# Kernel tuning notes

Hardware: AMD Instinct MI355X
Metric: run time of the kernel (lower is better)

Reference implementation:

```python
import jax, jax.numpy as jnp
import numpy as np

DT = 0.1
K = 262144


def _skew(v):
    # v: [k,3] -> [k,3,3]
    x, y, z = v[..., 0], v[..., 1], v[..., 2]
    O = jnp.zeros_like(x)
    return jnp.stack([
        jnp.stack([O, -z, y], -1),
        jnp.stack([z, O, -x], -1),
        jnp.stack([-y, x, O], -1)], -2)


def _se3_exp(t):
    # t: [k,6] twist = [rho(linear), phi(angular)] -> (R [k,3,3], p [k,3])
    rho, phi = t[:, :3], t[:, 3:]
    th2 = jnp.sum(phi * phi, -1)
    small = th2 < 1e-8
    th2s = jnp.where(small, 1.0, th2)        # safe denominator
    th = jnp.sqrt(th2s)
    A = jnp.where(small, 1.0 - th2 / 6.0, jnp.sin(th) / th)
    B = jnp.where(small, 0.5 - th2 / 24.0, (1.0 - jnp.cos(th)) / th2s)
    C = jnp.where(small, 1.0 / 6.0 - th2 / 120.0, (th - jnp.sin(th)) / (th2s * th))
    S = _skew(phi)
    S2 = S @ S
    I = jnp.eye(3, dtype=t.dtype)
    R = I + A[:, None, None] * S + B[:, None, None] * S2
    V = I + B[:, None, None] * S + C[:, None, None] * S2
    p = jnp.einsum('kij,kj->ki', V, rho)
    return R, p


def _adjoint(R, p):
    # SE3 adjoint for twist order [linear, angular]: [[R, [p]x R],[0, R]]
    top = jnp.concatenate([R, _skew(p) @ R], -1)
    bot = jnp.concatenate([jnp.zeros_like(R), R], -1)
    return jnp.concatenate([top, bot], -2)  # [k,6,6]


def setup_inputs() -> dict:
    key = jax.random.key(0)
    ks = jax.random.split(key, 8)
    s = jax.random.normal(ks[0], (K, 1, 18), dtype=jnp.float32) * 0.1
    # state layout: [pos(3), rot(9), twist(6)]; rotation must be a valid R (identity, as in fake_state)
    s = s.at[:, :, 3:12].set(jnp.eye(3, dtype=jnp.float32).reshape(9))
    a = jax.random.normal(ks[1], (K, 1, 6), dtype=jnp.float32) * 0.1
    h0 = jnp.zeros((1, K, 12), dtype=jnp.float32)
    W_ih = jax.random.normal(ks[2], (12, 21), dtype=jnp.float32) / np.sqrt(21)
    W_hh = jax.random.normal(ks[3], (12, 12), dtype=jnp.float32) / np.sqrt(12)
    W1 = jax.random.normal(ks[4], (128, 12), dtype=jnp.float32) / np.sqrt(12)
    W2 = jax.random.normal(ks[5], (128, 128), dtype=jnp.float32) / np.sqrt(128)
    W3 = jax.random.normal(ks[6], (6, 128), dtype=jnp.float32) / np.sqrt(128)
    return {"s": s, "a": a, "h0": h0, "W_ih": W_ih, "W_hh": W_hh, "W1": W1, "W2": W2, "W3": W3}


def reference(s, a, h0, W_ih, W_hh, W1, W2, W3):
    k = s.shape[0]
    # RNN input: pose-rot+vel (cols 3:) concat action -> [k, 21] (tau=1)
    x = jnp.concatenate([s[:, :, 3:], a], -1)[:, 0]
    h1 = jnp.tanh(x @ W_ih.T + h0[0] @ W_hh.T)          # [k,12] single RNN step, no bias
    hN = h1[None]                                        # [1,k,12]
    lrelu = lambda z: jnp.where(z >= 0, z, 0.1 * z)
    dv = lrelu(lrelu(h1 @ W1.T) @ W2.T) @ W3.T           # [k,6]
    v = s[:, -1, -6:]                                    # body twist
    p = s[:, -1, :3]
    R = s[:, -1, 3:12].reshape(k, 3, 3)
    # SE3 integration: M_next = M_current @ Exp(v*dt)
    Re, pe = _se3_exp(v * DT)
    R_next = R @ Re
    p_next = jnp.einsum('kij,kj->ki', R, pe) + p
    # M_next^-1
    Rinv = jnp.swapaxes(R_next, -1, -2)
    pinv = -jnp.einsum('kij,kj->ki', Rinv, p_next)
    # velocity update through adjoints
    vI = jnp.einsum('kij,kj->ki', _adjoint(R, p), v)
    v_next = jnp.einsum('kij,kj->ki', _adjoint(Rinv, pinv), vI + dv)
    s_next = jnp.concatenate([p_next, R_next.reshape(k, 9), v_next], -1)[:, None, :]
    return s_next, hN, dv
```

## Files before the change

### kernel.cpp

```cpp
#include <hip/hip_runtime.h>
#include <math.h>

typedef __attribute__((ext_vector_type(8))) short short8;
typedef __attribute__((ext_vector_type(4))) float f32x4;

#define DT_STEP 0.1f

static __device__ __forceinline__ unsigned bf16rne(float f) {
    unsigned u = __builtin_bit_cast(unsigned, f);
    return (u + 0x7fffu + ((u >> 16) & 1u)) >> 16;
}
static __device__ __forceinline__ unsigned short bf16pk1(float f) {
    unsigned r;
    asm("v_cvt_pk_bf16_f32 %0, %1, %1" : "=v"(r) : "v"(f));
    return (unsigned short)r;
}
static __device__ __forceinline__ unsigned bf16pk2(float lo, float hi) {
    unsigned r;
    asm("v_cvt_pk_bf16_f32 %0, %1, %2" : "=v"(r) : "v"(lo), "v"(hi));
    return r;
}
static __device__ __forceinline__ float tanh_fast(float v) {
    float e = __expf(2.0f * v);
    return 1.0f - 2.0f / (e + 1.0f);
}

static __device__ __forceinline__ void mm3(const float* A, const float* B, float* C) {
#pragma unroll
    for (int i = 0; i < 3; ++i)
#pragma unroll
        for (int j = 0; j < 3; ++j)
            C[i * 3 + j] = A[i * 3 + 0] * B[0 * 3 + j] + A[i * 3 + 1] * B[1 * 3 + j] + A[i * 3 + 2] * B[2 * 3 + j];
}
static __device__ __forceinline__ void mv3(const float* A, const float* x, float* y) {
#pragma unroll
    for (int i = 0; i < 3; ++i) y[i] = A[i * 3 + 0] * x[0] + A[i * 3 + 1] * x[1] + A[i * 3 + 2] * x[2];
}
static __device__ __forceinline__ void mtv3(const float* A, const float* x, float* y) {
#pragma unroll
    for (int i = 0; i < 3; ++i) y[i] = A[0 * 3 + i] * x[0] + A[1 * 3 + i] * x[1] + A[2 * 3 + i] * x[2];
}
static __device__ __forceinline__ void cross3(const float* p, const float* u, float* y) {
    y[0] = p[1] * u[2] - p[2] * u[1];
    y[1] = p[2] * u[0] - p[0] * u[2];
    y[2] = p[0] * u[1] - p[1] * u[0];
}

__global__ __launch_bounds__(256)
void weights_prep(const float* __restrict__ W1, const float* __restrict__ W2,
                  const float* __restrict__ W3, unsigned short* __restrict__ ws) {
    int i = blockIdx.x * 256 + threadIdx.x;
    if (i < 4096) {
        int n = i >> 5, k = i & 31;
        ws[i] = (k < 12) ? (unsigned short)bf16rne(W1[n * 12 + k]) : (unsigned short)0;
    } else if (i < 20480) {
        ws[i] = (unsigned short)bf16rne(W2[i - 4096]);
    } else if (i < 22528) {
        int j = i - 20480;
        int jj = j & 7;
        int l = (j >> 3) & 15;
        int kl = j >> 7;
        int k = kl * 8 + jj;
        ws[i] = (l < 6) ? (unsigned short)bf16rne(W3[l * 128 + k]) : (unsigned short)0;
    }
}

__global__ __launch_bounds__(256, 2)
void auv_mfma4_kernel(const float* __restrict__ s, const float* __restrict__ a,
                      const float* __restrict__ h0, const float* __restrict__ W_ih,
                      const float* __restrict__ W_hh, const unsigned short* __restrict__ Wbf,
                      float* __restrict__ out, int K)
{
    __shared__ __align__(16) char lds[4][18432];
    const int tid  = threadIdx.x;
    const int wid  = tid >> 6;
    const int lane = tid & 63;
    const int l15  = lane & 15;
    const int lg   = lane >> 4;

    char* base = &lds[wid][0];
    char* h1t  = base;
    char* l12  = base + 2048;
    char* dvt  = h1t;

    const unsigned short* W1A = Wbf;
    const unsigned short* W2B = Wbf + 4096;
    const unsigned short* W3B = Wbf + 20480;

    const int e_raw = blockIdx.x * 256 + wid * 64 + lane;
    const int e  = e_raw < K ? e_raw : K - 1;
    const bool live = e_raw < K;

    const float* srow = s  + (size_t)e * 18;
    const float* arow = a  + (size_t)e * 6;
    const float* hrow = h0 + (size_t)e * 12;

    float xv[21];
#pragma unroll
    for (int i = 0; i < 15; ++i) xv[i] = srow[3 + i];
#pragma unroll
    for (int i = 0; i < 6; ++i)  xv[15 + i] = arow[i];
    float h0v[12];
#pragma unroll
    for (int i = 0; i < 12; ++i) h0v[i] = hrow[i];

    float h1v[12];
#pragma unroll
    for (int j = 0; j < 12; ++j) {
        float acc = 0.f;
        const float* wih = W_ih + j * 21;
#pragma unroll
        for (int i = 0; i < 21; ++i) acc = fmaf(wih[i], xv[i], acc);
        const float* whh = W_hh + j * 12;
#pragma unroll
        for (int i = 0; i < 12; ++i) acc = fmaf(whh[i], h0v[i], acc);
        h1v[j] = tanh_fast(acc);
    }

    if (live) {
        float4* h4 = (float4*)(out + (size_t)K * 18 + (size_t)e * 12);
        h4[0] = make_float4(h1v[0], h1v[1], h1v[2], h1v[3]);
        h4[1] = make_float4(h1v[4], h1v[5], h1v[6], h1v[7]);
        h4[2] = make_float4(h1v[8], h1v[9], h1v[10], h1v[11]);
    }

    {
        unsigned p0 = bf16pk2(h1v[0], h1v[1]);
        unsigned p1 = bf16pk2(h1v[2], h1v[3]);
        unsigned p2 = bf16pk2(h1v[4], h1v[5]);
        unsigned p3 = bf16pk2(h1v[6], h1v[7]);
        unsigned p4 = bf16pk2(h1v[8], h1v[9]);
        unsigned p5 = bf16pk2(h1v[10], h1v[11]);
        int rq = (lane & 1) << 4;
        *(uint4*)(h1t + lane * 32 + (0 ^ rq))  = make_uint4(p0, p1, p2, p3);
        *(uint4*)(h1t + lane * 32 + (16 ^ rq)) = make_uint4(p4, p5, 0u, 0u);
    }
    asm volatile("s_waitcnt lgkmcnt(0)" ::: "memory");
    __builtin_amdgcn_sched_barrier(0);

    const short8 zfrag = {0, 0, 0, 0, 0, 0, 0, 0};

    short8 af1[4];
#pragma unroll
    for (int rt = 0; rt < 4; ++rt) {
        af1[rt] = zfrag;
        if (lg < 2) {
            int row = rt * 16 + l15;
            af1[rt] = __builtin_bit_cast(short8,
                *(const uint4*)(h1t + row * 32 + ((lg * 16) ^ ((row & 1) << 4))));
        }
    }
#pragma unroll 1
    for (int nt = 0; nt < 8; ++nt) {
        short8 b1 = __builtin_bit_cast(short8,
            *(const uint4*)(W1A + ((nt * 16 + l15) * 32 + lg * 8)));
#pragma unroll
        for (int rt = 0; rt < 4; ++rt) {
            f32x4 z = {0.f, 0.f, 0.f, 0.f};
            f32x4 c1 = __builtin_amdgcn_mfma_f32_16x16x32_bf16(af1[rt], b1, z, 0, 0, 0);
#pragma unroll
            for (int r = 0; r < 4; ++r) {
                int row = rt * 16 + lg * 4 + r;
                float v = c1[r];
                v = fmaxf(v, 0.1f * v);
                *(unsigned short*)(l12 + row * 256 +
                    (((nt * 16 + l15) * 2) ^ ((row & 15) << 4))) = bf16pk1(v);
            }
        }
    }
    asm volatile("s_waitcnt lgkmcnt(0)" ::: "memory");
    __builtin_amdgcn_sched_barrier(0);

    short8 af2[4][4];
#pragma unroll
    for (int rt = 0; rt < 4; ++rt)
#pragma unroll
        for (int kt = 0; kt < 4; ++kt) {
            int row = rt * 16 + l15;
            af2[rt][kt] = __builtin_bit_cast(short8,
                *(const uint4*)(l12 + row * 256 + ((kt * 64 + lg * 16) ^ ((row & 15) << 4))));
        }
    asm volatile("s_waitcnt lgkmcnt(0)" ::: "memory");
    __builtin_amdgcn_sched_barrier(0);

    short8 bfr[4];
#pragma unroll
    for (int kt = 0; kt < 4; ++kt)
        bfr[kt] = __builtin_bit_cast(short8,
            *(const uint4*)(W2B + (l15 * 128 + kt * 32 + lg * 8)));

#pragma unroll 1
    for (int nt = 0; nt < 8; ++nt) {
        short8 bnext[4];
        if (nt < 7) {
#pragma unroll
            for (int kt = 0; kt < 4; ++kt)
                bnext[kt] = __builtin_bit_cast(short8,
                    *(const uint4*)(W2B + (((nt + 1) * 16 + l15) * 128 + kt * 32 + lg * 8)));
        }
#pragma unroll
        for (int rt = 0; rt < 4; ++rt) {
            f32x4 c2 = {0.f, 0.f, 0.f, 0.f};
#pragma unroll
            for (int kt = 0; kt < 4; ++kt)
                c2 = __builtin_amdgcn_mfma_f32_16x16x32_bf16(af2[rt][kt], bfr[kt], c2, 0, 0, 0);
#pragma unroll
            for (int r = 0; r < 4; ++r) {
                int row = rt * 16 + lg * 4 + r;
                float v = c2[r];
                v = fmaxf(v, 0.1f * v);
                *(unsigned short*)(l12 + row * 256 +
                    (((nt * 16 + l15) * 2) ^ ((row & 15) << 4))) = bf16pk1(v);
            }
        }
#pragma unroll
        for (int kt = 0; kt < 4; ++kt) bfr[kt] = bnext[kt];
    }
    asm volatile("s_waitcnt lgkmcnt(0)" ::: "memory");
    __builtin_amdgcn_sched_barrier(0);

    short8 af3[4][4];
#pragma unroll
    for (int rt = 0; rt < 4; ++rt)
#pragma unroll
        for (int kt = 0; kt < 4; ++kt) {
            int row = rt * 16 + l15;
            af3[rt][kt] = __builtin_bit_cast(short8,
                *(const uint4*)(l12 + row * 256 + ((kt * 64 + lg * 16) ^ ((row & 15) << 4))));
        }
    asm volatile("s_waitcnt lgkmcnt(0)" ::: "memory");
    __builtin_amdgcn_sched_barrier(0);

    f32x4 c3[4];
#pragma unroll
    for (int rt = 0; rt < 4; ++rt) c3[rt] = (f32x4){0.f, 0.f, 0.f, 0.f};
#pragma unroll
    for (int kt = 0; kt < 4; ++kt) {
        short8 b3 = __builtin_bit_cast(short8,
            *(const uint4*)(W3B + (((kt * 4 + lg) * 16 + l15) * 8)));
#pragma unroll
        for (int rt = 0; rt < 4; ++rt)
            c3[rt] = __builtin_amdgcn_mfma_f32_16x16x32_bf16(af3[rt][kt], b3, c3[rt], 0, 0, 0);
    }

    float dvv[6];
    if (l15 < 6) {
#pragma unroll
        for (int rt = 0; rt < 4; ++rt)
#pragma unroll
            for (int r = 0; r < 4; ++r) {
                int row = rt * 16 + lg * 4 + r;
                *(float*)(dvt + row * 32 + l15 * 4) = c3[rt][r];
            }
    }
    asm volatile("s_waitcnt lgkmcnt(0)" ::: "memory");
    __builtin_amdgcn_sched_barrier(0);
    {
        const float* dr = (const float*)(dvt + lane * 32);
        dvv[0] = dr[0]; dvv[1] = dr[1]; dvv[2] = dr[2];
        dvv[3] = dr[3]; dvv[4] = dr[4]; dvv[5] = dr[5];
    }
    asm volatile("s_waitcnt lgkmcnt(0)" ::: "memory");
    __builtin_amdgcn_sched_barrier(0);

    float sv[18];
#pragma unroll
    for (int i = 0; i < 18; ++i) sv[i] = srow[i];
    const float* v = &sv[12];
    const float* p = &sv[0];
    const float* R = &sv[3];

    float rho[3] = {v[0] * DT_STEP, v[1] * DT_STEP, v[2] * DT_STEP};
    float phi[3] = {v[3] * DT_STEP, v[4] * DT_STEP, v[5] * DT_STEP};
    float th2 = phi[0] * phi[0] + phi[1] * phi[1] + phi[2] * phi[2];

    float A, B, C;
    if (th2 < 1e-8f) {
        A = 1.0f - th2 * (1.0f / 6.0f);
        B = 0.5f - th2 * (1.0f / 24.0f);
        C = (1.0f / 6.0f) - th2 * (1.0f / 120.0f);
    } else {
        float th = sqrtf(th2);
        float sn = sinf(th), cs = cosf(th);
        A = sn / th;
        B = (1.0f - cs) / th2;
        C = (th - sn) / (th2 * th);
    }

    float S[9] = {0.f, -phi[2], phi[1], phi[2], 0.f, -phi[0], -phi[1], phi[0], 0.f};
    float S2[9];
    mm3(S, S, S2);

    float Re[9], V[9];
#pragma unroll
    for (int i = 0; i < 9; ++i) {
        float I = (i == 0 || i == 4 || i == 8) ? 1.0f : 0.0f;
        Re[i] = I + A * S[i] + B * S2[i];
        V[i]  = I + B * S[i] + C * S2[i];
    }

    float pe[3];
    mv3(V, rho, pe);
    float Rn[9];
    mm3(R, Re, Rn);
    float pn[3];
    mv3(R, pe, pn);
    pn[0] += p[0]; pn[1] += p[1]; pn[2] += p[2];

    float pinv[3];
    mtv3(Rn, pn, pinv);
    pinv[0] = -pinv[0]; pinv[1] = -pinv[1]; pinv[2] = -pinv[2];

    float Rvl[3], Rva[3];
    mv3(R, &v[0], Rvl);
    mv3(R, &v[3], Rva);
    float px[3];
    cross3(p, Rva, px);
    float u6[6];
    u6[0] = Rvl[0] + px[0] + dvv[0];
    u6[1] = Rvl[1] + px[1] + dvv[1];
    u6[2] = Rvl[2] + px[2] + dvv[2];
    u6[3] = Rva[0] + dvv[3];
    u6[4] = Rva[1] + dvv[4];
    u6[5] = Rva[2] + dvv[5];

    float Rul[3], Rua[3];
    mtv3(Rn, &u6[0], Rul);
    mtv3(Rn, &u6[3], Rua);
    float pxu[3];
    cross3(pinv, Rua, pxu);
    float vn[6];
    vn[0] = Rul[0] + pxu[0];
    vn[1] = Rul[1] + pxu[1];
    vn[2] = Rul[2] + pxu[2];
    vn[3] = Rua[0];
    vn[4] = Rua[1];
    vn[5] = Rua[2];

    if (live) {
        float* s_next = out + (size_t)e * 18;
        s_next[0] = pn[0]; s_next[1] = pn[1]; s_next[2] = pn[2];
#pragma unroll
        for (int i = 0; i < 9; ++i) s_next[3 + i] = Rn[i];
#pragma unroll
        for (int i = 0; i < 6; ++i) s_next[12 + i] = vn[i];

        float* dvo = out + (size_t)K * 30 + (size_t)e * 6;
#pragma unroll
        for (int r = 0; r < 6; ++r) dvo[r] = dvv[r];
    }
}

extern "C" void kernel_launch(void* const* d_in, const int* in_sizes, int n_in,
                              void* d_out, int out_size, void* d_ws, size_t ws_size,
                              hipStream_t stream) {
    const float* s    = (const float*)d_in[0];
    const float* a    = (const float*)d_in[1];
    const float* h0   = (const float*)d_in[2];
    const float* W_ih = (const float*)d_in[3];
    const float* W_hh = (const float*)d_in[4];
    const float* W1   = (const float*)d_in[5];
    const float* W2   = (const float*)d_in[6];
    const float* W3   = (const float*)d_in[7];

    int K = in_sizes[0] / 18;
    unsigned short* ws = (unsigned short*)d_ws;

    weights_prep<<<(22528 + 255) / 256, 256, 0, stream>>>(W1, W2, W3, ws);

    int grid = (K + 255) / 256;
    auv_mfma4_kernel<<<grid, 256, 0, stream>>>(s, a, h0, W_ih, W_hh, ws,
                                               (float*)d_out, K);
}
```

Before: 56.81 us.

## Process 32 rows per wave to halve registers and LDS, raise occupancy

Each wave now handles 32 elements instead of 64: two lanes share an element for the RNN and h1 stores, and the MLP tiles drop from 4 to 2 row tiles. LDS per wave is halved and launch bounds go from 2 to 4 blocks per CU, with twice as many blocks launched. The RNN step is computed redundantly by both half-waves, and the SE3 tail runs on only half the lanes. The aim is more resident waves to hide memory latency, at the cost of lower per-wave MFMA utilisation and weight reloads spread over more waves.

```diff
diff --git a/kernel.cpp b/kernel.cpp
--- a/kernel.cpp
+++ b/kernel.cpp
@@ -65,29 +65,31 @@
     }
 }
 
-__global__ __launch_bounds__(256, 2)
-void auv_mfma4_kernel(const float* __restrict__ s, const float* __restrict__ a,
+__global__ __launch_bounds__(256, 4)
+void auv_mfma5_kernel(const float* __restrict__ s, const float* __restrict__ a,
                       const float* __restrict__ h0, const float* __restrict__ W_ih,
                       const float* __restrict__ W_hh, const unsigned short* __restrict__ Wbf,
                       float* __restrict__ out, int K)
 {
-    __shared__ __align__(16) char lds[4][18432];
+    __shared__ __align__(16) char lds[4][9216];
     const int tid  = threadIdx.x;
     const int wid  = tid >> 6;
     const int lane = tid & 63;
     const int l15  = lane & 15;
     const int lg   = lane >> 4;
+    const int el   = lane & 31;
+    const int half = lane >> 5;
 
     char* base = &lds[wid][0];
     char* h1t  = base;
-    char* l12  = base + 2048;
+    char* l12  = base + 1024;
     char* dvt  = h1t;
 
     const unsigned short* W1A = Wbf;
     const unsigned short* W2B = Wbf + 4096;
     const unsigned short* W3B = Wbf + 20480;
 
-    const int e_raw = blockIdx.x * 256 + wid * 64 + lane;
+    const int e_raw = blockIdx.x * 128 + wid * 32 + el;
     const int e  = e_raw < K ? e_raw : K - 1;
     const bool live = e_raw < K;
 
@@ -119,30 +121,33 @@
 
     if (live) {
         float4* h4 = (float4*)(out + (size_t)K * 18 + (size_t)e * 12);
-        h4[0] = make_float4(h1v[0], h1v[1], h1v[2], h1v[3]);
-        h4[1] = make_float4(h1v[4], h1v[5], h1v[6], h1v[7]);
-        h4[2] = make_float4(h1v[8], h1v[9], h1v[10], h1v[11]);
+        if (half == 0) {
+            h4[0] = make_float4(h1v[0], h1v[1], h1v[2], h1v[3]);
+            h4[1] = make_float4(h1v[4], h1v[5], h1v[6], h1v[7]);
+        } else {
+            h4[2] = make_float4(h1v[8], h1v[9], h1v[10], h1v[11]);
+        }
     }
 
     {
-        unsigned p0 = bf16pk2(h1v[0], h1v[1]);
-        unsigned p1 = bf16pk2(h1v[2], h1v[3]);
-        unsigned p2 = bf16pk2(h1v[4], h1v[5]);
-        unsigned p3 = bf16pk2(h1v[6], h1v[7]);
-        unsigned p4 = bf16pk2(h1v[8], h1v[9]);
-        unsigned p5 = bf16pk2(h1v[10], h1v[11]);
-        int rq = (lane & 1) << 4;
-        *(uint4*)(h1t + lane * 32 + (0 ^ rq))  = make_uint4(p0, p1, p2, p3);
-        *(uint4*)(h1t + lane * 32 + (16 ^ rq)) = make_uint4(p4, p5, 0u, 0u);
+        int rq = (el & 1) << 4;
+        if (half == 0) {
+            uint4 q = make_uint4(bf16pk2(h1v[0], h1v[1]), bf16pk2(h1v[2], h1v[3]),
+                                 bf16pk2(h1v[4], h1v[5]), bf16pk2(h1v[6], h1v[7]));
+            *(uint4*)(h1t + el * 32 + (0 ^ rq)) = q;
+        } else {
+            uint4 q = make_uint4(bf16pk2(h1v[8], h1v[9]), bf16pk2(h1v[10], h1v[11]), 0u, 0u);
+            *(uint4*)(h1t + el * 32 + (16 ^ rq)) = q;
+        }
     }
     asm volatile("s_waitcnt lgkmcnt(0)" ::: "memory");
     __builtin_amdgcn_sched_barrier(0);
 
     const short8 zfrag = {0, 0, 0, 0, 0, 0, 0, 0};
 
-    short8 af1[4];
-#pragma unroll
-    for (int rt = 0; rt < 4; ++rt) {
+    short8 af1[2];
+#pragma unroll
+    for (int rt = 0; rt < 2; ++rt) {
         af1[rt] = zfrag;
         if (lg < 2) {
             int row = rt * 16 + l15;
@@ -155,7 +160,7 @@
         short8 b1 = __builtin_bit_cast(short8,
             *(const uint4*)(W1A + ((nt * 16 + l15) * 32 + lg * 8)));
 #pragma unroll
-        for (int rt = 0; rt < 4; ++rt) {
+        for (int rt = 0; rt < 2; ++rt) {
             f32x4 z = {0.f, 0.f, 0.f, 0.f};
             f32x4 c1 = __builtin_amdgcn_mfma_f32_16x16x32_bf16(af1[rt], b1, z, 0, 0, 0);
 #pragma unroll
@@ -171,9 +176,9 @@
     asm volatile("s_waitcnt lgkmcnt(0)" ::: "memory");
     __builtin_amdgcn_sched_barrier(0);
 
-    short8 af2[4][4];
-#pragma unroll
-    for (int rt = 0; rt < 4; ++rt)
+    short8 af2[2][4];
+#pragma unroll
+    for (int rt = 0; rt < 2; ++rt)
 #pragma unroll
         for (int kt = 0; kt < 4; ++kt) {
             int row = rt * 16 + l15;
@@ -199,7 +204,7 @@
                     *(const uint4*)(W2B + (((nt + 1) * 16 + l15) * 128 + kt * 32 + lg * 8)));
         }
 #pragma unroll
-        for (int rt = 0; rt < 4; ++rt) {
+        for (int rt = 0; rt < 2; ++rt) {
             f32x4 c2 = {0.f, 0.f, 0.f, 0.f};
 #pragma unroll
             for (int kt = 0; kt < 4; ++kt)
@@ -219,9 +224,9 @@
     asm volatile("s_waitcnt lgkmcnt(0)" ::: "memory");
     __builtin_amdgcn_sched_barrier(0);
 
-    short8 af3[4][4];
-#pragma unroll
-    for (int rt = 0; rt < 4; ++rt)
+    short8 af3[2][4];
+#pragma unroll
+    for (int rt = 0; rt < 2; ++rt)
 #pragma unroll
         for (int kt = 0; kt < 4; ++kt) {
             int row = rt * 16 + l15;
@@ -231,22 +236,21 @@
     asm volatile("s_waitcnt lgkmcnt(0)" ::: "memory");
     __builtin_amdgcn_sched_barrier(0);
 
-    f32x4 c3[4];
-#pragma unroll
-    for (int rt = 0; rt < 4; ++rt) c3[rt] = (f32x4){0.f, 0.f, 0.f, 0.f};
+    f32x4 c3[2];
+    c3[0] = (f32x4){0.f, 0.f, 0.f, 0.f};
+    c3[1] = (f32x4){0.f, 0.f, 0.f, 0.f};
 #pragma unroll
     for (int kt = 0; kt < 4; ++kt) {
         short8 b3 = __builtin_bit_cast(short8,
             *(const uint4*)(W3B + (((kt * 4 + lg) * 16 + l15) * 8)));
 #pragma unroll
-        for (int rt = 0; rt < 4; ++rt)
+        for (int rt = 0; rt < 2; ++rt)
             c3[rt] = __builtin_amdgcn_mfma_f32_16x16x32_bf16(af3[rt][kt], b3, c3[rt], 0, 0, 0);
     }
 
-    float dvv[6];
     if (l15 < 6) {
 #pragma unroll
-        for (int rt = 0; rt < 4; ++rt)
+        for (int rt = 0; rt < 2; ++rt)
 #pragma unroll
             for (int r = 0; r < 4; ++r) {
                 int row = rt * 16 + lg * 4 + r;
@@ -255,99 +259,102 @@
     }
     asm volatile("s_waitcnt lgkmcnt(0)" ::: "memory");
     __builtin_amdgcn_sched_barrier(0);
+    float dvv[6];
     {
-        const float* dr = (const float*)(dvt + lane * 32);
+        const float* dr = (const float*)(dvt + el * 32);
         dvv[0] = dr[0]; dvv[1] = dr[1]; dvv[2] = dr[2];
         dvv[3] = dr[3]; dvv[4] = dr[4]; dvv[5] = dr[5];
     }
     asm volatile("s_waitcnt lgkmcnt(0)" ::: "memory");
     __builtin_amdgcn_sched_barrier(0);
 
-    float sv[18];
-#pragma unroll
-    for (int i = 0; i < 18; ++i) sv[i] = srow[i];
-    const float* v = &sv[12];
-    const float* p = &sv[0];
-    const float* R = &sv[3];
-
-    float rho[3] = {v[0] * DT_STEP, v[1] * DT_STEP, v[2] * DT_STEP};
-    float phi[3] = {v[3] * DT_STEP, v[4] * DT_STEP, v[5] * DT_STEP};
-    float th2 = phi[0] * phi[0] + phi[1] * phi[1] + phi[2] * phi[2];
-
-    float A, B, C;
-    if (th2 < 1e-8f) {
-        A = 1.0f - th2 * (1.0f / 6.0f);
-        B = 0.5f - th2 * (1.0f / 24.0f);
-        C = (1.0f / 6.0f) - th2 * (1.0f / 120.0f);
-    } else {
-        float th = sqrtf(th2);
-        float sn = sinf(th), cs = cosf(th);
-        A = sn / th;
-        B = (1.0f - cs) / th2;
-        C = (th - sn) / (th2 * th);
-    }
-
-    float S[9] = {0.f, -phi[2], phi[1], phi[2], 0.f, -phi[0], -phi[1], phi[0], 0.f};
-    float S2[9];
-    mm3(S, S, S2);
-
-    float Re[9], V[9];
-#pragma unroll
-    for (int i = 0; i < 9; ++i) {
-        float I = (i == 0 || i == 4 || i == 8) ? 1.0f : 0.0f;
-        Re[i] = I + A * S[i] + B * S2[i];
-        V[i]  = I + B * S[i] + C * S2[i];
-    }
-
-    float pe[3];
-    mv3(V, rho, pe);
-    float Rn[9];
-    mm3(R, Re, Rn);
-    float pn[3];
-    mv3(R, pe, pn);
-    pn[0] += p[0]; pn[1] += p[1]; pn[2] += p[2];
-
-    float pinv[3];
-    mtv3(Rn, pn, pinv);
-    pinv[0] = -pinv[0]; pinv[1] = -pinv[1]; pinv[2] = -pinv[2];
-
-    float Rvl[3], Rva[3];
-    mv3(R, &v[0], Rvl);
-    mv3(R, &v[3], Rva);
-    float px[3];
-    cross3(p, Rva, px);
-    float u6[6];
-    u6[0] = Rvl[0] + px[0] + dvv[0];
-    u6[1] = Rvl[1] + px[1] + dvv[1];
-    u6[2] = Rvl[2] + px[2] + dvv[2];
-    u6[3] = Rva[0] + dvv[3];
-    u6[4] = Rva[1] + dvv[4];
-    u6[5] = Rva[2] + dvv[5];
-
-    float Rul[3], Rua[3];
-    mtv3(Rn, &u6[0], Rul);
-    mtv3(Rn, &u6[3], Rua);
-    float pxu[3];
-    cross3(pinv, Rua, pxu);
-    float vn[6];
-    vn[0] = Rul[0] + pxu[0];
-    vn[1] = Rul[1] + pxu[1];
-    vn[2] = Rul[2] + pxu[2];
-    vn[3] = Rua[0];
-    vn[4] = Rua[1];
-    vn[5] = Rua[2];
-
-    if (live) {
-        float* s_next = out + (size_t)e * 18;
-        s_next[0] = pn[0]; s_next[1] = pn[1]; s_next[2] = pn[2];
-#pragma unroll
-        for (int i = 0; i < 9; ++i) s_next[3 + i] = Rn[i];
-#pragma unroll
-        for (int i = 0; i < 6; ++i) s_next[12 + i] = vn[i];
-
-        float* dvo = out + (size_t)K * 30 + (size_t)e * 6;
-#pragma unroll
-        for (int r = 0; r < 6; ++r) dvo[r] = dvv[r];
+    if (lane < 32) {
+        float sv[18];
+#pragma unroll
+        for (int i = 0; i < 18; ++i) sv[i] = srow[i];
+        const float* v = &sv[12];
+        const float* p = &sv[0];
+        const float* R = &sv[3];
+
+        float rho[3] = {v[0] * DT_STEP, v[1] * DT_STEP, v[2] * DT_STEP};
+        float phi[3] = {v[3] * DT_STEP, v[4] * DT_STEP, v[5] * DT_STEP};
+        float th2 = phi[0] * phi[0] + phi[1] * phi[1] + phi[2] * phi[2];
+
+        float A, B, C;
+        if (th2 < 1e-8f) {
+            A = 1.0f - th2 * (1.0f / 6.0f);
+            B = 0.5f - th2 * (1.0f / 24.0f);
+            C = (1.0f / 6.0f) - th2 * (1.0f / 120.0f);
+        } else {
+            float th = sqrtf(th2);
+            float sn = sinf(th), cs = cosf(th);
+            A = sn / th;
+            B = (1.0f - cs) / th2;
+            C = (th - sn) / (th2 * th);
+        }
+
+        float S[9] = {0.f, -phi[2], phi[1], phi[2], 0.f, -phi[0], -phi[1], phi[0], 0.f};
+        float S2[9];
+        mm3(S, S, S2);
+
+        float Re[9], V[9];
+#pragma unroll
+        for (int i = 0; i < 9; ++i) {
+            float I = (i == 0 || i == 4 || i == 8) ? 1.0f : 0.0f;
+            Re[i] = I + A * S[i] + B * S2[i];
+            V[i]  = I + B * S[i] + C * S2[i];
+        }
+
+        float pe[3];
+        mv3(V, rho, pe);
+        float Rn[9];
+        mm3(R, Re, Rn);
+        float pn[3];
+        mv3(R, pe, pn);
+        pn[0] += p[0]; pn[1] += p[1]; pn[2] += p[2];
+
+        float pinv[3];
+        mtv3(Rn, pn, pinv);
+        pinv[0] = -pinv[0]; pinv[1] = -pinv[1]; pinv[2] = -pinv[2];
+
+        float Rvl[3], Rva[3];
+        mv3(R, &v[0], Rvl);
+        mv3(R, &v[3], Rva);
+        float px[3];
+        cross3(p, Rva, px);
+        float u6[6];
+        u6[0] = Rvl[0] + px[0] + dvv[0];
+        u6[1] = Rvl[1] + px[1] + dvv[1];
+        u6[2] = Rvl[2] + px[2] + dvv[2];
+        u6[3] = Rva[0] + dvv[3];
+        u6[4] = Rva[1] + dvv[4];
+        u6[5] = Rva[2] + dvv[5];
+
+        float Rul[3], Rua[3];
+        mtv3(Rn, &u6[0], Rul);
+        mtv3(Rn, &u6[3], Rua);
+        float pxu[3];
+        cross3(pinv, Rua, pxu);
+        float vn[6];
+        vn[0] = Rul[0] + pxu[0];
+        vn[1] = Rul[1] + pxu[1];
+        vn[2] = Rul[2] + pxu[2];
+        vn[3] = Rua[0];
+        vn[4] = Rua[1];
+        vn[5] = Rua[2];
+
+        if (live) {
+            float* s_next = out + (size_t)e * 18;
+            s_next[0] = pn[0]; s_next[1] = pn[1]; s_next[2] = pn[2];
+#pragma unroll
+            for (int i = 0; i < 9; ++i) s_next[3 + i] = Rn[i];
+#pragma unroll
+            for (int i = 0; i < 6; ++i) s_next[12 + i] = vn[i];
+
+            float* dvo = out + (size_t)K * 30 + (size_t)e * 6;
+#pragma unroll
+            for (int r = 0; r < 6; ++r) dvo[r] = dvv[r];
+        }
     }
 }
 
@@ -368,7 +375,7 @@
 
     weights_prep<<<(22528 + 255) / 256, 256, 0, stream>>>(W1, W2, W3, ws);
 
-    int grid = (K + 255) / 256;
-    auv_mfma4_kernel<<<grid, 256, 0, stream>>>(s, a, h0, W_ih, W_hh, ws,
+    int grid = (K + 127) / 128;
+    auv_mfma5_kernel<<<grid, 256, 0, stream>>>(s, a, h0, W_ih, W_hh, ws,
                                                (float*)d_out, K);
 }
```

Measured after the change: 65.09 us. 14.6% more time.

## Use one-wave blocks, hoist weight loads, overlap SE3 math with MLP

Applied to the files above, without the earlier changes.

Moves from 256-thread blocks (four waves sharing a partitioned LDS array) to 64-thread single-wave blocks, each owning its own LDS region, with launch bounds targeting 3 blocks. W2 and W3 B-fragments are now loaded early so their latency hides behind other work. The SE3 integration runs before the final MFMA stage and reuses state values already held in registers instead of reloading the row. Most manual waitcnt/sched barriers are dropped in favour of compiler scheduling plus one s_barrier, which raises register pressure and relies on the compiler to order LDS accesses correctly.

```diff
diff --git a/kernel.cpp b/kernel.cpp
--- a/kernel.cpp
+++ b/kernel.cpp
@@ -65,29 +65,26 @@
     }
 }
 
-__global__ __launch_bounds__(256, 2)
-void auv_mfma4_kernel(const float* __restrict__ s, const float* __restrict__ a,
-                      const float* __restrict__ h0, const float* __restrict__ W_ih,
-                      const float* __restrict__ W_hh, const unsigned short* __restrict__ Wbf,
-                      float* __restrict__ out, int K)
+__global__ __launch_bounds__(64, 3)
+void auv_mfma10_kernel(const float* __restrict__ s, const float* __restrict__ a,
+                       const float* __restrict__ h0, const float* __restrict__ W_ih,
+                       const float* __restrict__ W_hh, const unsigned short* __restrict__ Wbf,
+                       float* __restrict__ out, int K)
 {
-    __shared__ __align__(16) char lds[4][18432];
-    const int tid  = threadIdx.x;
-    const int wid  = tid >> 6;
-    const int lane = tid & 63;
+    __shared__ __align__(16) char lds[18432];
+    const int lane = threadIdx.x & 63;
     const int l15  = lane & 15;
     const int lg   = lane >> 4;
 
-    char* base = &lds[wid][0];
-    char* h1t  = base;
-    char* l12  = base + 2048;
-    char* dvt  = h1t;
+    char* l12 = &lds[0];
+    char* h1t = &lds[16384];
+    char* dvt = &lds[0];
 
     const unsigned short* W1A = Wbf;
     const unsigned short* W2B = Wbf + 4096;
     const unsigned short* W3B = Wbf + 20480;
 
-    const int e_raw = blockIdx.x * 256 + wid * 64 + lane;
+    const int e_raw = blockIdx.x * 64 + lane;
     const int e  = e_raw < K ? e_raw : K - 1;
     const bool live = e_raw < K;
 
@@ -95,6 +92,8 @@
     const float* arow = a  + (size_t)e * 6;
     const float* hrow = h0 + (size_t)e * 12;
 
+    float pv3[3];
+    pv3[0] = srow[0]; pv3[1] = srow[1]; pv3[2] = srow[2];
     float xv[21];
 #pragma unroll
     for (int i = 0; i < 15; ++i) xv[i] = srow[3 + i];
@@ -123,6 +122,12 @@
         h4[1] = make_float4(h1v[4], h1v[5], h1v[6], h1v[7]);
         h4[2] = make_float4(h1v[8], h1v[9], h1v[10], h1v[11]);
     }
+
+    short8 bfr[4];
+#pragma unroll
+    for (int kt = 0; kt < 4; ++kt)
+        bfr[kt] = __builtin_bit_cast(short8,
+            *(const uint4*)(W2B + (l15 * 128 + kt * 32 + lg * 8)));
 
     {
         unsigned p0 = bf16pk2(h1v[0], h1v[1]);
@@ -135,8 +140,6 @@
         *(uint4*)(h1t + lane * 32 + (0 ^ rq))  = make_uint4(p0, p1, p2, p3);
         *(uint4*)(h1t + lane * 32 + (16 ^ rq)) = make_uint4(p4, p5, 0u, 0u);
     }
-    asm volatile("s_waitcnt lgkmcnt(0)" ::: "memory");
-    __builtin_amdgcn_sched_barrier(0);
 
     const short8 zfrag = {0, 0, 0, 0, 0, 0, 0, 0};
 
@@ -168,8 +171,6 @@
             }
         }
     }
-    asm volatile("s_waitcnt lgkmcnt(0)" ::: "memory");
-    __builtin_amdgcn_sched_barrier(0);
 
     short8 af2[4][4];
 #pragma unroll
@@ -180,14 +181,12 @@
             af2[rt][kt] = __builtin_bit_cast(short8,
                 *(const uint4*)(l12 + row * 256 + ((kt * 64 + lg * 16) ^ ((row & 15) << 4))));
         }
-    asm volatile("s_waitcnt lgkmcnt(0)" ::: "memory");
-    __builtin_amdgcn_sched_barrier(0);
-
-    short8 bfr[4];
+
+    short8 b3f[4];
 #pragma unroll
     for (int kt = 0; kt < 4; ++kt)
-        bfr[kt] = __builtin_bit_cast(short8,
-            *(const uint4*)(W2B + (l15 * 128 + kt * 32 + lg * 8)));
+        b3f[kt] = __builtin_bit_cast(short8,
+            *(const uint4*)(W3B + (((kt * 4 + lg) * 16 + l15) * 8)));
 
 #pragma unroll 1
     for (int nt = 0; nt < 8; ++nt) {
@@ -216,8 +215,6 @@
 #pragma unroll
         for (int kt = 0; kt < 4; ++kt) bfr[kt] = bnext[kt];
     }
-    asm volatile("s_waitcnt lgkmcnt(0)" ::: "memory");
-    __builtin_amdgcn_sched_barrier(0);
 
     short8 af3[4][4];
 #pragma unroll
@@ -228,19 +225,64 @@
             af3[rt][kt] = __builtin_bit_cast(short8,
                 *(const uint4*)(l12 + row * 256 + ((kt * 64 + lg * 16) ^ ((row & 15) << 4))));
         }
-    asm volatile("s_waitcnt lgkmcnt(0)" ::: "memory");
-    __builtin_amdgcn_sched_barrier(0);
+
+    const float* v = &xv[9];
+    const float* p = pv3;
+    const float* R = &xv[0];
+
+    float Rn[9], pn[3], pinv[3], Rvl[3], Rva[3], px[3];
+    {
+        float rho[3] = {v[0] * DT_STEP, v[1] * DT_STEP, v[2] * DT_STEP};
+        float phi[3] = {v[3] * DT_STEP, v[4] * DT_STEP, v[5] * DT_STEP};
+        float th2 = phi[0] * phi[0] + phi[1] * phi[1] + phi[2] * phi[2];
+
+        float A, B, C;
+        if (th2 < 1e-8f) {
+            A = 1.0f - th2 * (1.0f / 6.0f);
+            B = 0.5f - th2 * (1.0f / 24.0f);
+            C = (1.0f / 6.0f) - th2 * (1.0f / 120.0f);
+        } else {
+            float th = sqrtf(th2);
+            float sn = sinf(th), cs = cosf(th);
+            A = sn / th;
+            B = (1.0f - cs) / th2;
+            C = (th - sn) / (th2 * th);
+        }
+
+        float S[9] = {0.f, -phi[2], phi[1], phi[2], 0.f, -phi[0], -phi[1], phi[0], 0.f};
+        float S2[9];
+        mm3(S, S, S2);
+
+        float Re[9], V[9];
+#pragma unroll
+        for (int i = 0; i < 9; ++i) {
+            float I = (i == 0 || i == 4 || i == 8) ? 1.0f : 0.0f;
+            Re[i] = I + A * S[i] + B * S2[i];
+            V[i]  = I + B * S[i] + C * S2[i];
+        }
+
+        float pe[3];
+        mv3(V, rho, pe);
+        mm3(R, Re, Rn);
+        mv3(R, pe, pn);
+        pn[0] += p[0]; pn[1] += p[1]; pn[2] += p[2];
+
+        mtv3(Rn, pn, pinv);
+        pinv[0] = -pinv[0]; pinv[1] = -pinv[1]; pinv[2] = -pinv[2];
+
+        mv3(R, &v[0], Rvl);
+        mv3(R, &v[3], Rva);
+        cross3(p, Rva, px);
+    }
 
     f32x4 c3[4];
 #pragma unroll
     for (int rt = 0; rt < 4; ++rt) c3[rt] = (f32x4){0.f, 0.f, 0.f, 0.f};
 #pragma unroll
     for (int kt = 0; kt < 4; ++kt) {
-        short8 b3 = __builtin_bit_cast(short8,
-            *(const uint4*)(W3B + (((kt * 4 + lg) * 16 + l15) * 8)));
 #pragma unroll
         for (int rt = 0; rt < 4; ++rt)
-            c3[rt] = __builtin_amdgcn_mfma_f32_16x16x32_bf16(af3[rt][kt], b3, c3[rt], 0, 0, 0);
+            c3[rt] = __builtin_amdgcn_mfma_f32_16x16x32_bf16(af3[rt][kt], b3f[kt], c3[rt], 0, 0, 0);
     }
 
     float dvv[6];
@@ -253,69 +295,13 @@
                 *(float*)(dvt + row * 32 + l15 * 4) = c3[rt][r];
             }
     }
-    asm volatile("s_waitcnt lgkmcnt(0)" ::: "memory");
-    __builtin_amdgcn_sched_barrier(0);
+    __builtin_amdgcn_s_barrier();
     {
         const float* dr = (const float*)(dvt + lane * 32);
         dvv[0] = dr[0]; dvv[1] = dr[1]; dvv[2] = dr[2];
         dvv[3] = dr[3]; dvv[4] = dr[4]; dvv[5] = dr[5];
     }
-    asm volatile("s_waitcnt lgkmcnt(0)" ::: "memory");
-    __builtin_amdgcn_sched_barrier(0);
-
-    float sv[18];
-#pragma unroll
-    for (int i = 0; i < 18; ++i) sv[i] = srow[i];
-    const float* v = &sv[12];
-    const float* p = &sv[0];
-    const float* R = &sv[3];
-
-    float rho[3] = {v[0] * DT_STEP, v[1] * DT_STEP, v[2] * DT_STEP};
-    float phi[3] = {v[3] * DT_STEP, v[4] * DT_STEP, v[5] * DT_STEP};
-    float th2 = phi[0] * phi[0] + phi[1] * phi[1] + phi[2] * phi[2];
-
-    float A, B, C;
-    if (th2 < 1e-8f) {
-        A = 1.0f - th2 * (1.0f / 6.0f);
-        B = 0.5f - th2 * (1.0f / 24.0f);
-        C = (1.0f / 6.0f) - th2 * (1.0f / 120.0f);
-    } else {
-        float th = sqrtf(th2);
-        float sn = sinf(th), cs = cosf(th);
-        A = sn / th;
-        B = (1.0f - cs) / th2;
-        C = (th - sn) / (th2 * th);
-    }
-
-    float S[9] = {0.f, -phi[2], phi[1], phi[2], 0.f, -phi[0], -phi[1], phi[0], 0.f};
-    float S2[9];
-    mm3(S, S, S2);
-
-    float Re[9], V[9];
-#pragma unroll
-    for (int i = 0; i < 9; ++i) {
-        float I = (i == 0 || i == 4 || i == 8) ? 1.0f : 0.0f;
-        Re[i] = I + A * S[i] + B * S2[i];
-        V[i]  = I + B * S[i] + C * S2[i];
-    }
-
-    float pe[3];
-    mv3(V, rho, pe);
-    float Rn[9];
-    mm3(R, Re, Rn);
-    float pn[3];
-    mv3(R, pe, pn);
-    pn[0] += p[0]; pn[1] += p[1]; pn[2] += p[2];
-
-    float pinv[3];
-    mtv3(Rn, pn, pinv);
-    pinv[0] = -pinv[0]; pinv[1] = -pinv[1]; pinv[2] = -pinv[2];
-
-    float Rvl[3], Rva[3];
-    mv3(R, &v[0], Rvl);
-    mv3(R, &v[3], Rva);
-    float px[3];
-    cross3(p, Rva, px);
+
     float u6[6];
     u6[0] = Rvl[0] + px[0] + dvv[0];
     u6[1] = Rvl[1] + px[1] + dvv[1];
@@ -368,7 +354,7 @@
 
     weights_prep<<<(22528 + 255) / 256, 256, 0, stream>>>(W1, W2, W3, ws);
 
-    int grid = (K + 255) / 256;
-    auv_mfma4_kernel<<<grid, 256, 0, stream>>>(s, a, h0, W_ih, W_hh, ws,
+    int grid = (K + 63) / 64;
+    auv_mfma10_kernel<<<grid, 64, 0, stream>>>(s, a, h0, W_ih, W_hh, ws,
                                                (float*)d_out, K);
 }
```

After: 52.72 us (median of 2 runs). -7.2%, faster.
